# Kernel optimization log

Hardware: AMD Instinct MI355X
Metric: run time of the kernel (lower is better)

Reference implementation:

```python
import jax, jax.numpy as jnp
import numpy as np

POOL = 16
HEADS = 32
DP = 128  # dim_pairwise
DIM = 768


def relative_shift(t):
    # t: (..., seq_len, dim); pad/reshape/slice trick exactly as torch version
    *lead, s, d = t.shape
    t = jnp.pad(t, [(0, 0)] * len(lead) + [(0, 0), (1, 0)])
    t = t.reshape(*lead, d + 1, s)
    return t[..., 1:, :].reshape(*lead, s, d)


def setup_inputs() -> dict:
    key = jax.random.key(0)
    ks = jax.random.split(key, 8)
    b, n = 1, 1024
    seq, p = n * POOL, 2 * n
    s = 0.02
    return {
        "single": jax.random.normal(ks[0], (b, seq, DIM), jnp.float32),
        "rel_pos_feats": jax.random.normal(ks[1], (p, DIM), jnp.float32),
        "w_qk": jax.random.normal(ks[2], (2 * HEADS * DP, DIM), jnp.float32) * s,
        "w_outer": jax.random.normal(ks[3], (2 * DP, DIM), jnp.float32) * s,
        "w_pair": jax.random.normal(ks[4], (DP, HEADS), jnp.float32) * s,
        "b_pair": jnp.zeros((DP,), jnp.float32),
        "w_rel": jax.random.normal(ks[5], (HEADS * DP, DIM), jnp.float32) * s,
        "b_rel": jnp.zeros((HEADS * DP,), jnp.float32),
        "qk_rel_pos_bias": jax.random.normal(ks[6], (2, 1, 1, HEADS, DP), jnp.float32) * s,
    }


def reference(single, rel_pos_feats, w_qk, w_outer, w_pair, b_pair, w_rel, b_rel, qk_rel_pos_bias):
    b, seq, d = single.shape
    n = seq // POOL
    # avg pool over non-overlapping windows: b (n pool) d -> b n d
    single = single.reshape(b, n, POOL, d).mean(axis=2)

    # q, k projections + head split
    qk = single @ w_qk.T                      # (b, n, 2*h*dp)
    q, k = jnp.split(qk, 2, axis=-1)
    q = q.reshape(b, n, HEADS, DP)
    k = k.reshape(b, n, HEADS, DP)
    sim = jnp.einsum('bihd,bjhd->bijh', q, k)  # (b, n, n, h)

    # relative position bias path
    rel_enc = (rel_pos_feats @ w_rel.T + b_rel).reshape(-1, HEADS, DP)  # (p, h, dp)
    q_bias, k_bias = qk_rel_pos_bias[0], qk_rel_pos_bias[1]             # (1,1,h,dp)
    rel_q = relative_shift(jnp.einsum('bnhd,phd->bnph', q + q_bias, rel_enc))
    rel_k = relative_shift(jnp.einsum('bnhd,phd->bnph', k + k_bias, rel_enc))
    p = rel_q.shape[2]
    crop = (p - n) // 2
    rel_q = rel_q[:, :, crop:crop + n, :]
    rel_k = rel_k[:, :, crop:crop + n, :]
    rel_sim = (rel_q + jnp.transpose(rel_k, (0, 2, 1, 3))) * 0.5  # add('b i j d, b j i d -> b i j d')
    sim = sim + rel_sim

    pairwise_from_sim = sim @ w_pair.T + b_pair  # (b, n, n, dp)

    # outer-sum construction
    outer = jax.nn.gelu(single, approximate=False) @ w_outer.T  # (b, n, 2*dp)
    outer_q, outer_k = jnp.split(outer, 2, axis=-1)
    outer_sum = outer_q[:, :, None, :] + outer_k[:, None, :, :]  # (b, n, n, dp)

    return outer_sum + pairwise_from_sim
```

## Files before the change

### kernel.cpp

```cpp
#include <hip/hip_runtime.h>
#include <cmath>

typedef __bf16 bf16x8 __attribute__((ext_vector_type(8)));
typedef float f32x4 __attribute__((ext_vector_type(4)));

__device__ __forceinline__ float b2f(unsigned short u) {
  union { unsigned int i; float f; } v;
  v.i = ((unsigned int)u) << 16;
  return v.f;
}
__device__ __forceinline__ unsigned short f2b(float f) {
  union { float f; unsigned int i; } v;
  v.f = f;
  unsigned int i = v.i;
  return (unsigned short)((i + 0x7FFFu + ((i >> 16) & 1u)) >> 16);
}

__global__ __launch_bounds__(256) void k_cast(const float* __restrict__ src,
                                              unsigned short* __restrict__ dst,
                                              int n4) {
  int gid = blockIdx.x * 256 + threadIdx.x;
  if (gid >= n4) return;
  float4 v = *(const float4*)(src + (long)gid * 4);
  uint2 r;
  r.x = (unsigned int)f2b(v.x) | ((unsigned int)f2b(v.y) << 16);
  r.y = (unsigned int)f2b(v.z) | ((unsigned int)f2b(v.w) << 16);
  *(uint2*)(dst + (long)gid * 4) = r;
}

__global__ __launch_bounds__(256) void k_pool(const float* __restrict__ single,
                                              unsigned short* __restrict__ pooled,
                                              unsigned short* __restrict__ gpool) {
  int gid = blockIdx.x * 256 + threadIdx.x;
  int n = gid / 192;
  int dq = (gid - n * 192) * 4;
  const float* src = single + (long)n * (16 * 768) + dq;
  float s0 = 0.f, s1 = 0.f, s2 = 0.f, s3 = 0.f;
#pragma unroll
  for (int t = 0; t < 16; t++) {
    float4 u = *(const float4*)(src + t * 768);
    s0 += u.x; s1 += u.y; s2 += u.z; s3 += u.w;
  }
  float p0 = s0 * 0.0625f, p1 = s1 * 0.0625f, p2 = s2 * 0.0625f, p3 = s3 * 0.0625f;
  const float inv_sqrt2 = 0.70710678118654752f;
  float g0 = 0.5f * p0 * (1.f + erff(p0 * inv_sqrt2));
  float g1 = 0.5f * p1 * (1.f + erff(p1 * inv_sqrt2));
  float g2 = 0.5f * p2 * (1.f + erff(p2 * inv_sqrt2));
  float g3 = 0.5f * p3 * (1.f + erff(p3 * inv_sqrt2));
  long o = (long)n * 768 + dq;
  uint2 rp, rg;
  rp.x = (unsigned int)f2b(p0) | ((unsigned int)f2b(p1) << 16);
  rp.y = (unsigned int)f2b(p2) | ((unsigned int)f2b(p3) << 16);
  rg.x = (unsigned int)f2b(g0) | ((unsigned int)f2b(g1) << 16);
  rg.y = (unsigned int)f2b(g2) | ((unsigned int)f2b(g3) << 16);
  *(uint2*)(pooled + o) = rp;
  *(uint2*)(gpool + o) = rg;
}

template <class Epi>
__global__ __launch_bounds__(256) void gemm_bt(const unsigned short* __restrict__ A,
                                               const unsigned short* __restrict__ B,
                                               int K, long sA, long sB, Epi epi) {
  __shared__ __align__(16) unsigned short As[64][40];
  __shared__ __align__(16) unsigned short Bs[64][40];
  const int tid = threadIdx.x;
  const int lane = tid & 63;
  const int wave = tid >> 6;
  const int wm = wave >> 1;
  const int wn = wave & 1;
  const int z = blockIdx.z;
  const unsigned short* Ab = A + (long)z * sA;
  const unsigned short* Bb = B + (long)z * sB;
  const int m0 = blockIdx.x * 64;
  const int n0 = blockIdx.y * 64;
  const int lrow = tid >> 2;
  const int lcol = (tid & 3) * 8;
  const int frow = lane & 15;
  const int fk = (lane >> 4) * 8;

  f32x4 zero = {0.f, 0.f, 0.f, 0.f};
  f32x4 acc00 = zero, acc01 = zero, acc10 = zero, acc11 = zero;

  for (int k0 = 0; k0 < K; k0 += 32) {
    *(uint4*)(&As[lrow][lcol]) = *(const uint4*)(Ab + (long)(m0 + lrow) * K + k0 + lcol);
    *(uint4*)(&Bs[lrow][lcol]) = *(const uint4*)(Bb + (long)(n0 + lrow) * K + k0 + lcol);
    __syncthreads();
    bf16x8 a0 = *(const bf16x8*)(&As[wm * 32 + frow][fk]);
    bf16x8 a1 = *(const bf16x8*)(&As[wm * 32 + 16 + frow][fk]);
    bf16x8 b0 = *(const bf16x8*)(&Bs[wn * 32 + frow][fk]);
    bf16x8 b1 = *(const bf16x8*)(&Bs[wn * 32 + 16 + frow][fk]);
    acc00 = __builtin_amdgcn_mfma_f32_16x16x32_bf16(a0, b0, acc00, 0, 0, 0);
    acc01 = __builtin_amdgcn_mfma_f32_16x16x32_bf16(a0, b1, acc01, 0, 0, 0);
    acc10 = __builtin_amdgcn_mfma_f32_16x16x32_bf16(a1, b0, acc10, 0, 0, 0);
    acc11 = __builtin_amdgcn_mfma_f32_16x16x32_bf16(a1, b1, acc11, 0, 0, 0);
    __syncthreads();
  }
  const int em = m0 + wm * 32 + (lane >> 4) * 4;
  const int en = n0 + wn * 32 + (lane & 15);
#pragma unroll
  for (int r = 0; r < 4; r++) {
    epi(em + r,      en,      z, acc00[r]);
    epi(em + r,      en + 16, z, acc01[r]);
    epi(em + 16 + r, en,      z, acc10[r]);
    epi(em + 16 + r, en + 16, z, acc11[r]);
  }
}

struct EpiQK {
  unsigned short* q; unsigned short* k; unsigned short* qb; unsigned short* kb;
  const float* bias;
  __device__ void operator()(int m, int n, int z, float v) const {
    int co = n & 4095;
    int h = co >> 7, d = co & 127;
    long o = ((long)h * 1024 + m) * 128 + d;
    float bv = bias[n];
    if (n < 4096) { q[o] = f2b(v); qb[o] = f2b(v + bv); }
    else          { k[o] = f2b(v); kb[o] = f2b(v + bv); }
  }
};
struct EpiRel {
  unsigned short* rel; const float* brel;
  __device__ void operator()(int m, int n, int z, float v) const {
    int h = n >> 7, d = n & 127;
    rel[((long)h * 2048 + m) * 128 + d] = f2b(v + brel[n]);
  }
};
struct EpiOuter {
  float* oq; float* ok;
  __device__ void operator()(int m, int n, int z, float v) const {
    if (n < 128) oq[(long)m * 128 + n] = v;
    else         ok[(long)m * 128 + (n - 128)] = v;
  }
};
struct EpiSimC {
  unsigned short* S;
  __device__ void operator()(int m, int n, int z, float v) const {
    S[((long)m * 32 + z) * 1024 + n] = f2b(v);
  }
};
struct EpiRqC {
  unsigned short* R;
  __device__ void operator()(int m, int n, int z, float v) const {
    R[((long)z * 256 + m) * 1024 + n] = f2b(v);
  }
};
struct EpiRkC {
  unsigned short* R;
  __device__ void operator()(int m, int n, int z, float v) const {
    R[((long)z * 320 + m) * 1024 + n] = f2b(v);
  }
};

__global__ __launch_bounds__(256) void k_final2(
    const unsigned short* __restrict__ S0,
    const unsigned short* __restrict__ Rq,
    const unsigned short* __restrict__ Rk,
    const float* __restrict__ oq,
    const float* __restrict__ okf,
    const float* __restrict__ wp,
    const float* __restrict__ bp,
    float* __restrict__ out,
    int i0, int ps_lo) {
  __shared__ __align__(16) unsigned short sl[32][72];
  __shared__ __align__(16) unsigned short rq_l[32][72];
  const int il = blockIdx.y;
  const int i  = i0 + il;
  const int j0 = blockIdx.x * 64;
  const int t  = threadIdx.x;
  const int h  = t >> 3;
  const int jj = (t & 7) * 8;

  const int p0  = (j0 * 32 + 18431) / 33;
  const int pcA = (p0 - 544) & ~7;
  for (int c = t; c < 288; c += 256) {
    int row = c / 9;
    int off = (c - row * 9) * 8;
    *(uint4*)(&rq_l[row][off]) =
        *(const uint4*)(Rq + ((long)row * 256 + il) * 1024 + pcA + off);
  }
  uint4 s0v = *(const uint4*)(S0 + ((long)il * 32 + h) * 1024 + j0 + jj);
  const int t2  = i * 32 + h + 18431;
  const int ps2 = t2 / 33;
  const int hs2 = t2 - ps2 * 33;
  uint4 rkv = {0u, 0u, 0u, 0u};
  if (hs2 < 32)
    rkv = *(const uint4*)(Rk + ((long)hs2 * 320 + (ps2 - ps_lo)) * 1024 + j0 + jj);
  __syncthreads();
  const unsigned short* s0p = (const unsigned short*)&s0v;
  const unsigned short* rkp = (const unsigned short*)&rkv;
#pragma unroll
  for (int e = 0; e < 8; e++) {
    const int j  = jj + e;
    const int t1 = (j0 + j) * 32 + h + 18431;
    const int ps1 = t1 / 33;
    const int hs1 = t1 - ps1 * 33;
    float rq = (hs1 < 32) ? b2f(rq_l[hs1][ps1 - 544 - pcA]) : 0.f;
    sl[h][j] = f2b(b2f(s0p[e]) + 0.5f * (rq + b2f(rkp[e])));
  }
  __syncthreads();
  const int lane = t & 63;
  const int wv = t >> 6;
  const int jbase = wv * 16;
  const int r16 = lane & 15;
  const int kq = lane >> 4;
  union { unsigned short u[8]; bf16x8 v; } af;
#pragma unroll
  for (int s = 0; s < 8; s++) af.u[s] = sl[kq * 8 + s][jbase + r16];
#pragma unroll
  for (int ct = 0; ct < 8; ct++) {
    const int c0 = ct * 16;
    union { unsigned short u[8]; bf16x8 v; } bfr;
#pragma unroll
    for (int s = 0; s < 8; s++) bfr.u[s] = f2b(wp[(c0 + r16) * 32 + kq * 8 + s]);
    f32x4 acc = {0.f, 0.f, 0.f, 0.f};
    acc = __builtin_amdgcn_mfma_f32_16x16x32_bf16(af.v, bfr.v, acc, 0, 0, 0);
    const int cD = c0 + r16;
    const float addc = oq[i * 128 + cD] + bp[cD];
#pragma unroll
    for (int r = 0; r < 4; r++) {
      const int j = j0 + jbase + kq * 4 + r;
      out[(long)i * 131072 + j * 128 + cD] = acc[r] + addc + okf[j * 128 + cD];
    }
  }
}

extern "C" void kernel_launch(void* const* d_in, const int* in_sizes, int n_in,
                              void* d_out, int out_size, void* d_ws, size_t ws_size,
                              hipStream_t stream) {
  (void)in_sizes; (void)n_in; (void)out_size; (void)ws_size;
  const float* single  = (const float*)d_in[0];
  const float* relfeat = (const float*)d_in[1];
  const float* w_qk    = (const float*)d_in[2];
  const float* w_outer = (const float*)d_in[3];
  const float* w_pair  = (const float*)d_in[4];
  const float* b_pair  = (const float*)d_in[5];
  const float* w_rel   = (const float*)d_in[6];
  const float* b_rel   = (const float*)d_in[7];
  const float* qk_bias = (const float*)d_in[8];
  float* out = (float*)d_out;
  char* ws = (char*)d_ws;

  unsigned short* pooled  = (unsigned short*)(ws + 0);
  unsigned short* gpool   = (unsigned short*)(ws + 1572864);
  unsigned short* q       = (unsigned short*)(ws + 3145728);
  unsigned short* k       = (unsigned short*)(ws + 11534336);
  unsigned short* qb      = (unsigned short*)(ws + 19922944);
  unsigned short* kb      = (unsigned short*)(ws + 28311552);
  unsigned short* rel     = (unsigned short*)(ws + 36700160);
  float*          oq      = (float*)(ws + 53477376);
  float*          okf     = (float*)(ws + 54001664);
  unsigned short* wqk_b   = (unsigned short*)(ws + 54525952);
  unsigned short* wrel_b  = (unsigned short*)(ws + 67108864);
  unsigned short* rfeat_b = (unsigned short*)(ws + 73400320);
  unsigned short* wout_b  = (unsigned short*)(ws + 76546048);
  unsigned short* S0c     = (unsigned short*)(ws + 76939264);
  unsigned short* Rqc     = (unsigned short*)(ws + 93716480);
  unsigned short* Rkc     = (unsigned short*)(ws + 110493696);

  k_cast<<<6144, 256, 0, stream>>>(w_qk,    wqk_b,   1572864);
  k_cast<<<3072, 256, 0, stream>>>(w_rel,   wrel_b,   786432);
  k_cast<<<1536, 256, 0, stream>>>(relfeat, rfeat_b,  393216);
  k_cast<<< 192, 256, 0, stream>>>(w_outer, wout_b,    49152);

  k_pool<<<768, 256, 0, stream>>>(single, pooled, gpool);
  gemm_bt<<<dim3(16, 128, 1), 256, 0, stream>>>(pooled, wqk_b, 768, 0L, 0L,
                                                EpiQK{q, k, qb, kb, qk_bias});
  gemm_bt<<<dim3(32, 64, 1), 256, 0, stream>>>(rfeat_b, wrel_b, 768, 0L, 0L,
                                               EpiRel{rel, b_rel});
  gemm_bt<<<dim3(16, 4, 1), 256, 0, stream>>>(gpool, wout_b, 768, 0L, 0L,
                                              EpiOuter{oq, okf});

  for (int ic = 0; ic < 4; ic++) {
    const int i0 = ic * 256;
    const int ps_lo = (32 * i0 + 18431) / 33;
    gemm_bt<<<dim3(4, 16, 32), 256, 0, stream>>>(q + (long)i0 * 128, k, 128,
                                                 131072L, 131072L, EpiSimC{S0c});
    gemm_bt<<<dim3(4, 16, 32), 256, 0, stream>>>(qb + (long)i0 * 128, rel + 69632,
                                                 128, 131072L, 262144L, EpiRqC{Rqc});
    gemm_bt<<<dim3(5, 16, 32), 256, 0, stream>>>(rel + (long)ps_lo * 128, kb, 128,
                                                 262144L, 131072L, EpiRkC{Rkc});
    k_final2<<<dim3(16, 256), 256, 0, stream>>>(S0c, Rqc, Rkc, oq, okf,
                                                w_pair, b_pair, out, i0, ps_lo);
  }
}
```

Measured before the change: 1.027 ms.

## Enlarge GEMM tiles to 128x128 with direct global-to-LDS loads, merge casts, single chunk

The generic bf16 GEMM moves from 64x64 to 128x128 block tiles, with each wave computing a 4x4 grid of MFMA fragments for more register reuse. Operands are staged with global_load_lds, which copies straight into shared memory, and the padded LDS rows are dropped. The four weight-cast launches are merged into one kernel. When the workspace is large enough, the pairwise stage runs as one chunk instead of four, cutting launch count. Risks are LDS bank conflicts from the unpadded layout, lower occupancy from the larger accumulator set, a larger workspace footprint, and a dependence on ws_size for which path runs.

```diff
diff --git a/kernel.cpp b/kernel.cpp
--- a/kernel.cpp
+++ b/kernel.cpp
@@ -16,16 +16,28 @@
   return (unsigned short)((i + 0x7FFFu + ((i >> 16) & 1u)) >> 16);
 }
 
-__global__ __launch_bounds__(256) void k_cast(const float* __restrict__ src,
-                                              unsigned short* __restrict__ dst,
-                                              int n4) {
+__device__ __forceinline__ void gld_lds16(const unsigned short* g, unsigned short* l) {
+  __builtin_amdgcn_global_load_lds(
+      (__attribute__((address_space(1))) void*)(void*)(g),
+      (__attribute__((address_space(3))) void*)(l), 16, 0, 0);
+}
+
+__global__ __launch_bounds__(256) void k_cast_all(
+    const float* __restrict__ s0, unsigned short* __restrict__ d0,
+    const float* __restrict__ s1, unsigned short* __restrict__ d1,
+    const float* __restrict__ s2, unsigned short* __restrict__ d2,
+    const float* __restrict__ s3, unsigned short* __restrict__ d3) {
   int gid = blockIdx.x * 256 + threadIdx.x;
-  if (gid >= n4) return;
-  float4 v = *(const float4*)(src + (long)gid * 4);
+  const float* s; unsigned short* d;
+  if (gid < 1572864)      { s = s0; d = d0; }
+  else if (gid < 2359296) { s = s1; d = d1; gid -= 1572864; }
+  else if (gid < 2752512) { s = s2; d = d2; gid -= 2359296; }
+  else                    { s = s3; d = d3; gid -= 2752512; }
+  float4 v = *(const float4*)(s + (long)gid * 4);
   uint2 r;
   r.x = (unsigned int)f2b(v.x) | ((unsigned int)f2b(v.y) << 16);
   r.y = (unsigned int)f2b(v.z) | ((unsigned int)f2b(v.w) << 16);
-  *(uint2*)(dst + (long)gid * 4) = r;
+  *(uint2*)(d + (long)gid * 4) = r;
 }
 
 __global__ __launch_bounds__(256) void k_pool(const float* __restrict__ single,
@@ -61,49 +73,56 @@
 __global__ __launch_bounds__(256) void gemm_bt(const unsigned short* __restrict__ A,
                                                const unsigned short* __restrict__ B,
                                                int K, long sA, long sB, Epi epi) {
-  __shared__ __align__(16) unsigned short As[64][40];
-  __shared__ __align__(16) unsigned short Bs[64][40];
+  __shared__ __align__(16) unsigned short As[128 * 32];
+  __shared__ __align__(16) unsigned short Bs[128 * 32];
   const int tid = threadIdx.x;
   const int lane = tid & 63;
-  const int wave = tid >> 6;
-  const int wm = wave >> 1;
-  const int wn = wave & 1;
+  const int w = tid >> 6;
+  const int wm = w >> 1;
+  const int wn = w & 1;
   const int z = blockIdx.z;
   const unsigned short* Ab = A + (long)z * sA;
   const unsigned short* Bb = B + (long)z * sB;
-  const int m0 = blockIdx.x * 64;
-  const int n0 = blockIdx.y * 64;
-  const int lrow = tid >> 2;
-  const int lcol = (tid & 3) * 8;
+  const int m0 = blockIdx.x * 128;
+  const int n0 = blockIdx.y * 128;
   const int frow = lane & 15;
   const int fk = (lane >> 4) * 8;
-
-  f32x4 zero = {0.f, 0.f, 0.f, 0.f};
-  f32x4 acc00 = zero, acc01 = zero, acc10 = zero, acc11 = zero;
+  const int r0 = tid >> 2;
+  const int c0 = (tid & 3) * 8;
+  f32x4 acc[4][4];
+#pragma unroll
+  for (int fm = 0; fm < 4; fm++)
+#pragma unroll
+    for (int fn = 0; fn < 4; fn++) acc[fm][fn] = (f32x4){0.f, 0.f, 0.f, 0.f};
 
   for (int k0 = 0; k0 < K; k0 += 32) {
-    *(uint4*)(&As[lrow][lcol]) = *(const uint4*)(Ab + (long)(m0 + lrow) * K + k0 + lcol);
-    *(uint4*)(&Bs[lrow][lcol]) = *(const uint4*)(Bb + (long)(n0 + lrow) * K + k0 + lcol);
+    gld_lds16(Ab + (long)(m0 + r0) * K + k0 + c0,       &As[(w * 64) * 8]);
+    gld_lds16(Ab + (long)(m0 + 64 + r0) * K + k0 + c0,  &As[(256 + w * 64) * 8]);
+    gld_lds16(Bb + (long)(n0 + r0) * K + k0 + c0,       &Bs[(w * 64) * 8]);
+    gld_lds16(Bb + (long)(n0 + 64 + r0) * K + k0 + c0,  &Bs[(256 + w * 64) * 8]);
     __syncthreads();
-    bf16x8 a0 = *(const bf16x8*)(&As[wm * 32 + frow][fk]);
-    bf16x8 a1 = *(const bf16x8*)(&As[wm * 32 + 16 + frow][fk]);
-    bf16x8 b0 = *(const bf16x8*)(&Bs[wn * 32 + frow][fk]);
-    bf16x8 b1 = *(const bf16x8*)(&Bs[wn * 32 + 16 + frow][fk]);
-    acc00 = __builtin_amdgcn_mfma_f32_16x16x32_bf16(a0, b0, acc00, 0, 0, 0);
-    acc01 = __builtin_amdgcn_mfma_f32_16x16x32_bf16(a0, b1, acc01, 0, 0, 0);
-    acc10 = __builtin_amdgcn_mfma_f32_16x16x32_bf16(a1, b0, acc10, 0, 0, 0);
-    acc11 = __builtin_amdgcn_mfma_f32_16x16x32_bf16(a1, b1, acc11, 0, 0, 0);
+    bf16x8 a[4], b[4];
+#pragma unroll
+    for (int f = 0; f < 4; f++) {
+      a[f] = *(const bf16x8*)&As[(wm * 64 + f * 16 + frow) * 32 + fk];
+      b[f] = *(const bf16x8*)&Bs[(wn * 64 + f * 16 + frow) * 32 + fk];
+    }
+#pragma unroll
+    for (int fm = 0; fm < 4; fm++)
+#pragma unroll
+      for (int fn = 0; fn < 4; fn++)
+        acc[fm][fn] = __builtin_amdgcn_mfma_f32_16x16x32_bf16(a[fm], b[fn], acc[fm][fn], 0, 0, 0);
     __syncthreads();
   }
-  const int em = m0 + wm * 32 + (lane >> 4) * 4;
-  const int en = n0 + wn * 32 + (lane & 15);
-#pragma unroll
-  for (int r = 0; r < 4; r++) {
-    epi(em + r,      en,      z, acc00[r]);
-    epi(em + r,      en + 16, z, acc01[r]);
-    epi(em + 16 + r, en,      z, acc10[r]);
-    epi(em + 16 + r, en + 16, z, acc11[r]);
-  }
+  const int er = (lane >> 4) * 4;
+  const int ec = lane & 15;
+#pragma unroll
+  for (int fm = 0; fm < 4; fm++)
+#pragma unroll
+    for (int fn = 0; fn < 4; fn++)
+#pragma unroll
+      for (int r = 0; r < 4; r++)
+        epi(m0 + wm * 64 + fm * 16 + er + r, n0 + wn * 64 + fn * 16 + ec, z, acc[fm][fn][r]);
 }
 
 struct EpiQK {
@@ -139,15 +158,15 @@
   }
 };
 struct EpiRqC {
-  unsigned short* R;
-  __device__ void operator()(int m, int n, int z, float v) const {
-    R[((long)z * 256 + m) * 1024 + n] = f2b(v);
+  unsigned short* R; int CH;
+  __device__ void operator()(int m, int n, int z, float v) const {
+    R[((long)z * CH + m) * 1024 + n] = f2b(v);
   }
 };
 struct EpiRkC {
-  unsigned short* R;
-  __device__ void operator()(int m, int n, int z, float v) const {
-    R[((long)z * 320 + m) * 1024 + n] = f2b(v);
+  unsigned short* R; int RR;
+  __device__ void operator()(int m, int n, int z, float v) const {
+    R[((long)z * RR + m) * 1024 + n] = f2b(v);
   }
 };
 
@@ -160,7 +179,7 @@
     const float* __restrict__ wp,
     const float* __restrict__ bp,
     float* __restrict__ out,
-    int i0, int ps_lo) {
+    int i0, int ps_lo, int CH, int RR) {
   __shared__ __align__(16) unsigned short sl[32][72];
   __shared__ __align__(16) unsigned short rq_l[32][72];
   const int il = blockIdx.y;
@@ -176,7 +195,7 @@
     int row = c / 9;
     int off = (c - row * 9) * 8;
     *(uint4*)(&rq_l[row][off]) =
-        *(const uint4*)(Rq + ((long)row * 256 + il) * 1024 + pcA + off);
+        *(const uint4*)(Rq + ((long)row * CH + il) * 1024 + pcA + off);
   }
   uint4 s0v = *(const uint4*)(S0 + ((long)il * 32 + h) * 1024 + j0 + jj);
   const int t2  = i * 32 + h + 18431;
@@ -184,7 +203,7 @@
   const int hs2 = t2 - ps2 * 33;
   uint4 rkv = {0u, 0u, 0u, 0u};
   if (hs2 < 32)
-    rkv = *(const uint4*)(Rk + ((long)hs2 * 320 + (ps2 - ps_lo)) * 1024 + j0 + jj);
+    rkv = *(const uint4*)(Rk + ((long)hs2 * RR + (ps2 - ps_lo)) * 1024 + j0 + jj);
   __syncthreads();
   const unsigned short* s0p = (const unsigned short*)&s0v;
   const unsigned short* rkp = (const unsigned short*)&rkv;
@@ -227,7 +246,7 @@
 extern "C" void kernel_launch(void* const* d_in, const int* in_sizes, int n_in,
                               void* d_out, int out_size, void* d_ws, size_t ws_size,
                               hipStream_t stream) {
-  (void)in_sizes; (void)n_in; (void)out_size; (void)ws_size;
+  (void)in_sizes; (void)n_in; (void)out_size;
   const float* single  = (const float*)d_in[0];
   const float* relfeat = (const float*)d_in[1];
   const float* w_qk    = (const float*)d_in[2];
@@ -253,33 +272,36 @@
   unsigned short* wrel_b  = (unsigned short*)(ws + 67108864);
   unsigned short* rfeat_b = (unsigned short*)(ws + 73400320);
   unsigned short* wout_b  = (unsigned short*)(ws + 76546048);
-  unsigned short* S0c     = (unsigned short*)(ws + 76939264);
-  unsigned short* Rqc     = (unsigned short*)(ws + 93716480);
-  unsigned short* Rkc     = (unsigned short*)(ws + 110493696);
-
-  k_cast<<<6144, 256, 0, stream>>>(w_qk,    wqk_b,   1572864);
-  k_cast<<<3072, 256, 0, stream>>>(w_rel,   wrel_b,   786432);
-  k_cast<<<1536, 256, 0, stream>>>(relfeat, rfeat_b,  393216);
-  k_cast<<< 192, 256, 0, stream>>>(w_outer, wout_b,    49152);
-
+
+  int nch, CH, RR;
+  if (ws_size >= 280u * 1024u * 1024u) { nch = 1; CH = 1024; RR = 1024; }
+  else                                 { nch = 4; CH = 256;  RR = 384;  }
+  unsigned short* S0c = (unsigned short*)(ws + 76939264);
+  unsigned short* Rqc = S0c + (long)CH * 32 * 1024;
+  unsigned short* Rkc = Rqc + (long)CH * 32 * 1024;
+
+  k_cast_all<<<10944, 256, 0, stream>>>(w_qk, wqk_b, w_rel, wrel_b,
+                                        relfeat, rfeat_b, w_outer, wout_b);
   k_pool<<<768, 256, 0, stream>>>(single, pooled, gpool);
-  gemm_bt<<<dim3(16, 128, 1), 256, 0, stream>>>(pooled, wqk_b, 768, 0L, 0L,
-                                                EpiQK{q, k, qb, kb, qk_bias});
-  gemm_bt<<<dim3(32, 64, 1), 256, 0, stream>>>(rfeat_b, wrel_b, 768, 0L, 0L,
+  gemm_bt<<<dim3(8, 64, 1), 256, 0, stream>>>(pooled, wqk_b, 768, 0L, 0L,
+                                              EpiQK{q, k, qb, kb, qk_bias});
+  gemm_bt<<<dim3(16, 32, 1), 256, 0, stream>>>(rfeat_b, wrel_b, 768, 0L, 0L,
                                                EpiRel{rel, b_rel});
-  gemm_bt<<<dim3(16, 4, 1), 256, 0, stream>>>(gpool, wout_b, 768, 0L, 0L,
-                                              EpiOuter{oq, okf});
-
-  for (int ic = 0; ic < 4; ic++) {
-    const int i0 = ic * 256;
+  gemm_bt<<<dim3(8, 2, 1), 256, 0, stream>>>(gpool, wout_b, 768, 0L, 0L,
+                                             EpiOuter{oq, okf});
+
+  for (int ic = 0; ic < nch; ic++) {
+    const int i0 = ic * CH;
     const int ps_lo = (32 * i0 + 18431) / 33;
-    gemm_bt<<<dim3(4, 16, 32), 256, 0, stream>>>(q + (long)i0 * 128, k, 128,
-                                                 131072L, 131072L, EpiSimC{S0c});
-    gemm_bt<<<dim3(4, 16, 32), 256, 0, stream>>>(qb + (long)i0 * 128, rel + 69632,
-                                                 128, 131072L, 262144L, EpiRqC{Rqc});
-    gemm_bt<<<dim3(5, 16, 32), 256, 0, stream>>>(rel + (long)ps_lo * 128, kb, 128,
-                                                 262144L, 131072L, EpiRkC{Rkc});
-    k_final2<<<dim3(16, 256), 256, 0, stream>>>(S0c, Rqc, Rkc, oq, okf,
-                                                w_pair, b_pair, out, i0, ps_lo);
-  }
-}
+    gemm_bt<<<dim3(CH / 128, 8, 32), 256, 0, stream>>>(q + (long)i0 * 128, k, 128,
+                                                       131072L, 131072L, EpiSimC{S0c});
+    gemm_bt<<<dim3(CH / 128, 8, 32), 256, 0, stream>>>(qb + (long)i0 * 128, rel + 69632,
+                                                       128, 131072L, 262144L,
+                                                       EpiRqC{Rqc, CH});
+    gemm_bt<<<dim3(RR / 128, 8, 32), 256, 0, stream>>>(rel + (long)ps_lo * 128, kb, 128,
+                                                       262144L, 131072L,
+                                                       EpiRkC{Rkc, RR});
+    k_final2<<<dim3(16, CH), 256, 0, stream>>>(S0c, Rqc, Rkc, oq, okf,
+                                               w_pair, b_pair, out, i0, ps_lo, CH, RR);
+  }
+}
```

Result: faster. 989.9 us (-3.7%).
